# Optimization experiments

Measured on AMD Instinct MI355X. Metric: run time of the kernel, lower is better.

Reference implementation:

```python
import jax, jax.numpy as jnp
import numpy as np

NQ = 4            # num_qubits
DIM = 2 ** NQ     # 16-dim complex state

def _rx(theta):
    c = jnp.cos(theta / 2.0); s = jnp.sin(theta / 2.0)
    return jnp.array([[c, -1j * s], [-1j * s, c]], dtype=jnp.complex64)

def _ry(theta):
    c = jnp.cos(theta / 2.0); s = jnp.sin(theta / 2.0)
    return jnp.array([[c, -s], [s, c]], dtype=jnp.complex64)

def _apply_1q(state, q, U):
    # state: [B, 16] complex; apply 2x2 unitary U on qubit q (qubit 0 = MSB)
    B = state.shape[0]
    st = state.reshape((B,) + (2,) * NQ)
    st = jnp.moveaxis(st, 1 + q, -1)
    st = st @ U.T
    st = jnp.moveaxis(st, -1, 1 + q)
    return st.reshape(B, DIM)

def _apply_cnot(state, c, t):
    # flip target qubit t where control qubit c == 1
    B = state.shape[0]
    st = state.reshape((B,) + (2,) * NQ)
    st = jnp.moveaxis(st, (1 + c, 1 + t), (-2, -1))
    st = jnp.stack([st[..., 0, :], st[..., 1, ::-1]], axis=-2)
    st = jnp.moveaxis(st, (-2, -1), (1 + c, 1 + t))
    return st.reshape(B, DIM)

def _circuit(state):
    rx1, ry1 = _rx(0.1), _ry(0.2)
    rx2, ry2 = _rx(0.3), _ry(0.4)
    for q in range(NQ):
        state = _apply_1q(state, q, rx1)
        state = _apply_1q(state, q, ry1)
    for q in range(NQ - 1):
        state = _apply_cnot(state, q, q + 1)
    for q in range(NQ):
        state = _apply_1q(state, q, rx2)
        state = _apply_1q(state, q, ry2)
    return state

def setup_inputs() -> dict:
    key = jax.random.key(0)
    ks = jax.random.split(key, 9)
    B = 65536
    return {
        'x':   jax.random.normal(ks[0], (B, 784), dtype=jnp.float32),
        'We1': jax.random.normal(ks[1], (784, 256), dtype=jnp.float32) * 0.05,
        'be1': jnp.zeros((256,), dtype=jnp.float32),
        'We2': jax.random.normal(ks[2], (256, 32), dtype=jnp.float32) * 0.05,
        'be2': jnp.zeros((32,), dtype=jnp.float32),
        'W1':  jax.random.normal(ks[3], (32, 128), dtype=jnp.float32) * 0.05,
        'b1':  jnp.zeros((128,), dtype=jnp.float32),
        'W2':  jax.random.normal(ks[4], (128, 10), dtype=jnp.float32) * 0.05,
        'b2':  jnp.zeros((10,), dtype=jnp.float32),
    }

def reference(x, We1, be1, We2, be2, W1, b1, W2, b2):
    # encoder: Linear(784,256) -> ReLU -> Linear(256,32) -> Tanh
    h = jax.nn.relu(x @ We1 + be1)
    enc = jnp.tanh(h @ We2 + be2)               # [B, 32]
    psi = (enc[:, :DIM] + 1j * enc[:, DIM:]).astype(jnp.complex64)
    norm = jnp.sqrt(jnp.sum(jnp.abs(psi) ** 2, axis=1, keepdims=True))
    psi = psi / norm
    psi = _circuit(psi)                          # [B, 16] complex
    feat = jnp.concatenate([psi.real, psi.imag], axis=1)  # [B, 32]
    # classifier: Linear(32,128) -> ReLU -> (Dropout=identity in eval) -> Linear(128,10)
    out = jax.nn.relu(feat @ W1 + b1) @ W2 + b2
    return out
```

## Files before the change

kernel.cpp:

```cpp
#include <hip/hip_runtime.h>
#include <stdint.h>

#define DEVINL __device__ __forceinline__

typedef short bf16x8 __attribute__((ext_vector_type(8)));
typedef float f32x4  __attribute__((ext_vector_type(4)));

DEVINL uint16_t f2bf(float f) {
    uint32_t u = __builtin_bit_cast(uint32_t, f);
    uint32_t r = u + 0x7fffu + ((u >> 16) & 1u);
    return (uint16_t)(r >> 16);
}

DEVINL f32x4 mfma16x16x32(bf16x8 a, bf16x8 b, f32x4 c) {
    return __builtin_amdgcn_mfma_f32_16x16x32_bf16(a, b, c, 0, 0, 0);
}

DEVINL void async_load16(const void* g, void* l) {
    __builtin_amdgcn_global_load_lds(
        (const __attribute__((address_space(1))) void*)g,
        (__attribute__((address_space(3))) void*)l, 16, 0, 0);
}

#define WS_WE1T 0
#define WS_WE2T 425984
#define WS_W1T  442368
#define WS_W2T  450560

__global__ __launch_bounds__(256) void prep_weights(
    const float* __restrict__ We1, const float* __restrict__ We2,
    const float* __restrict__ W1,  const float* __restrict__ W2,
    uint16_t* __restrict__ We1T, uint16_t* __restrict__ We2T,
    uint16_t* __restrict__ W1T,  uint16_t* __restrict__ W2T) {
    int tid = blockIdx.x * 256 + threadIdx.x;
    if (tid < 256 * 832) {
        int n = tid / 832, k = tid % 832;
        We1T[tid] = (k < 784) ? f2bf(We1[k * 256 + n]) : (uint16_t)0;
        return;
    }
    int t2 = tid - 256 * 832;
    if (t2 < 32 * 256) {
        int n = t2 / 256, k = t2 % 256;
        We2T[t2] = f2bf(We2[k * 32 + n]);
        return;
    }
    int t3 = t2 - 32 * 256;
    if (t3 < 128 * 32) {
        int n = t3 / 32, k = t3 % 32;
        W1T[t3] = f2bf(W1[k * 128 + n]);
        return;
    }
    int t4 = t3 - 128 * 32;
    if (t4 < 16 * 128) {
        int n = t4 / 128, k = t4 % 128;
        W2T[t4] = (n < 10) ? f2bf(W2[k * 10 + n]) : (uint16_t)0;
        return;
    }
}

DEVINL void apply_rx(float* sr, float* si, int bit, float c, float s) {
    #pragma unroll
    for (int i = 0; i < 16; i++) {
        if (!(i & bit)) {
            int j = i | bit;
            float r0 = sr[i], i0 = si[i], r1 = sr[j], i1 = si[j];
            sr[i] = c * r0 + s * i1;  si[i] = c * i0 - s * r1;
            sr[j] = c * r1 + s * i0;  si[j] = c * i1 - s * r0;
        }
    }
}
DEVINL void apply_ry(float* sr, float* si, int bit, float c, float s) {
    #pragma unroll
    for (int i = 0; i < 16; i++) {
        if (!(i & bit)) {
            int j = i | bit;
            float r0 = sr[i], i0 = si[i], r1 = sr[j], i1 = si[j];
            sr[i] = c * r0 - s * r1;  si[i] = c * i0 - s * i1;
            sr[j] = s * r0 + c * r1;  si[j] = s * i0 + c * i1;
        }
    }
}
DEVINL void apply_cnot(float* sr, float* si, int cb, int tb) {
    #pragma unroll
    for (int i = 0; i < 16; i++) {
        if ((i & cb) && !(i & tb)) {
            int j = i | tb;
            float tr = sr[i]; sr[i] = sr[j]; sr[j] = tr;
            float ti = si[i]; si[i] = si[j]; si[j] = ti;
        }
    }
}
DEVINL void circuit(float* sr, float* si) {
    const float C1 = 0.99875026039496628f, S1 = 0.04997916927067833f;
    const float C2 = 0.99500416527802582f, S2 = 0.09983341664682815f;
    const float C3 = 0.98877107793604227f, S3 = 0.14943813247359922f;
    const float C4 = 0.98006657784124163f, S4 = 0.19866933079506122f;
    #pragma unroll
    for (int q = 0; q < 4; q++) {
        int bit = 8 >> q;
        apply_rx(sr, si, bit, C1, S1);
        apply_ry(sr, si, bit, C2, S2);
    }
    apply_cnot(sr, si, 8, 4);
    apply_cnot(sr, si, 4, 2);
    apply_cnot(sr, si, 2, 1);
    #pragma unroll
    for (int q = 0; q < 4; q++) {
        int bit = 8 >> q;
        apply_rx(sr, si, bit, C3, S3);
        apply_ry(sr, si, bit, C4, S4);
    }
}

DEVINL void stage_B(const uint16_t* __restrict__ We1T, int k0, uint16_t* Bls, int t) {
    #pragma unroll
    for (int j = 0; j < 8; j++) {
        int g  = j * 256 + t;
        int br = g >> 3;
        int bc = ((g & 7) ^ (br & 7)) * 8;
        async_load16(We1T + (size_t)br * 832 + k0 + bc, &Bls[8 * g]);
    }
}

DEVINL void pack_A(const float4* va, uint16_t* Als, int ar, int ach0, int ach1) {
    union { uint4 u4; uint16_t us[8]; } p0, p1;
    p0.us[0] = f2bf(va[0].x); p0.us[1] = f2bf(va[0].y);
    p0.us[2] = f2bf(va[0].z); p0.us[3] = f2bf(va[0].w);
    p0.us[4] = f2bf(va[1].x); p0.us[5] = f2bf(va[1].y);
    p0.us[6] = f2bf(va[1].z); p0.us[7] = f2bf(va[1].w);
    p1.us[0] = f2bf(va[2].x); p1.us[1] = f2bf(va[2].y);
    p1.us[2] = f2bf(va[2].z); p1.us[3] = f2bf(va[2].w);
    p1.us[4] = f2bf(va[3].x); p1.us[5] = f2bf(va[3].y);
    p1.us[6] = f2bf(va[3].z); p1.us[7] = f2bf(va[3].w);
    *(uint4*)&Als[ar * 64 + ach0 * 8] = p0.u4;
    *(uint4*)&Als[ar * 64 + ach1 * 8] = p1.u4;
}

DEVINL void load_va(float4* va, const float* __restrict__ xrow, int k0, int ac) {
    #pragma unroll
    for (int j = 0; j < 4; j++) {
        int c = k0 + ac + j * 4;
        c = (c <= 780) ? c : 780;
        va[j] = *(const float4*)(xrow + c);
    }
}

DEVINL void compute_tile(const uint16_t* Als, const uint16_t* Bls,
                         f32x4 (&acc)[4][4], int w, int lm, int lq) {
    #pragma unroll
    for (int kk = 0; kk < 2; kk++) {
        bf16x8 afr[4], bfr[4];
        #pragma unroll
        for (int mi = 0; mi < 4; mi++) {
            int row = mi * 16 + lm;
            int ch  = (kk * 4 + lq) ^ (lm & 7);
            afr[mi] = *(const bf16x8*)&Als[row * 64 + ch * 8];
        }
        #pragma unroll
        for (int ni = 0; ni < 4; ni++) {
            int row = w * 64 + ni * 16 + lm;
            int ch  = (kk * 4 + lq) ^ (lm & 7);
            bfr[ni] = *(const bf16x8*)&Bls[row * 64 + ch * 8];
        }
        __builtin_amdgcn_s_setprio(1);
        #pragma unroll
        for (int mi = 0; mi < 4; mi++)
            #pragma unroll
            for (int ni = 0; ni < 4; ni++)
                acc[mi][ni] = mfma16x16x32(afr[mi], bfr[ni], acc[mi][ni]);
        __builtin_amdgcn_s_setprio(0);
    }
}

__global__ __launch_bounds__(256, 2) void fused_kernel(
    const float* __restrict__ x, const uint16_t* __restrict__ We1T,
    const float* __restrict__ be1,
    const uint16_t* __restrict__ We2T, const float* __restrict__ be2,
    const uint16_t* __restrict__ W1T, const float* __restrict__ b1,
    const uint16_t* __restrict__ W2T, const float* __restrict__ b2,
    float* __restrict__ out) {
    __shared__ __align__(16) char smem[81920];
    uint16_t* Htile = (uint16_t*)smem;
    float*    encls  = (float*)smem;
    uint16_t* featls = (uint16_t*)(smem + 8448);
    uint16_t* a1ls   = (uint16_t*)(smem + 13568);

    const int t = threadIdx.x;
    const int rowbase = blockIdx.x * 64;
    const int w  = t >> 6;
    const int l  = t & 63;
    const int lm = l & 15;
    const int lq = l >> 4;

    f32x4 acc[4][4] = {};

    const int ar = t >> 2;
    const int ac = (t & 3) * 16;
    const float* xrow = x + (size_t)(rowbase + ar) * 784;
    const int ach0 = ((t & 3) * 2)     ^ (ar & 7);
    const int ach1 = ((t & 3) * 2 + 1) ^ (ar & 7);

    float4 va[4];

    load_va(va, xrow, 0, ac);
    stage_B(We1T, 0, (uint16_t*)(smem + 8192), t);
    __builtin_amdgcn_sched_barrier(0);
    pack_A(va, (uint16_t*)smem, ar, ach0, ach1);
    load_va(va, xrow, 64, ac);
    asm volatile("s_waitcnt lgkmcnt(0)" ::: "memory");
    asm volatile("s_waitcnt vmcnt(4)" ::: "memory");
    __builtin_amdgcn_s_barrier();
    asm volatile("" ::: "memory");

    int cur = 0;
    for (int it = 0; it < 12; ++it) {
        char* bc = smem + cur * 40960;
        char* bn = smem + (cur ^ 1) * 40960;
        stage_B(We1T, (it + 1) * 64, (uint16_t*)(bn + 8192), t);
        __builtin_amdgcn_sched_barrier(0);
        pack_A(va, (uint16_t*)bn, ar, ach0, ach1);
        load_va(va, xrow, (it + 2) * 64, ac);
        compute_tile((const uint16_t*)bc, (const uint16_t*)(bc + 8192), acc, w, lm, lq);
        asm volatile("s_waitcnt lgkmcnt(0)" ::: "memory");
        asm volatile("s_waitcnt vmcnt(4)" ::: "memory");
        __builtin_amdgcn_s_barrier();
        asm volatile("" ::: "memory");
        cur ^= 1;
    }
    {
        char* bc = smem + cur * 40960;
        compute_tile((const uint16_t*)bc, (const uint16_t*)(bc + 8192), acc, w, lm, lq);
    }

    __syncthreads();

    #pragma unroll
    for (int ni = 0; ni < 4; ni++) {
        int n = w * 64 + ni * 16 + lm;
        float bias = be1[n];
        #pragma unroll
        for (int mi = 0; mi < 4; mi++) {
            #pragma unroll
            for (int i = 0; i < 4; i++) {
                int r = mi * 16 + lq * 4 + i;
                float v = acc[mi][ni][i] + bias;
                v = v > 0.f ? v : 0.f;
                Htile[r * 272 + n] = f2bf(v);
            }
        }
    }
    __syncthreads();

    f32x4 acc2[2] = {};
    #pragma unroll
    for (int k0 = 0; k0 < 256; k0 += 32) {
        bf16x8 af = *(const bf16x8*)&Htile[(w * 16 + lm) * 272 + k0 + lq * 8];
        #pragma unroll
        for (int ni = 0; ni < 2; ni++) {
            bf16x8 bf = *(const bf16x8*)&We2T[(ni * 16 + lm) * 256 + k0 + lq * 8];
            acc2[ni] = mfma16x16x32(af, bf, acc2[ni]);
        }
    }
    __syncthreads();

    #pragma unroll
    for (int ni = 0; ni < 2; ni++) {
        int col = ni * 16 + lm;
        float bias = be2[col];
        #pragma unroll
        for (int i = 0; i < 4; i++) {
            int r = w * 16 + lq * 4 + i;
            encls[r * 33 + col] = tanhf(acc2[ni][i] + bias);
        }
    }
    __syncthreads();

    if (t < 64) {
        float e[32];
        #pragma unroll
        for (int j = 0; j < 32; j++) e[j] = encls[t * 33 + j];
        float s = 0.f;
        #pragma unroll
        for (int j = 0; j < 32; j++) s += e[j] * e[j];
        float inv = 1.0f / sqrtf(s);
        float sr[16], si[16];
        #pragma unroll
        for (int i = 0; i < 16; i++) { sr[i] = e[i] * inv; si[i] = e[16 + i] * inv; }
        circuit(sr, si);
        #pragma unroll
        for (int i = 0; i < 16; i++) {
            featls[t * 40 + i]      = f2bf(sr[i]);
            featls[t * 40 + 16 + i] = f2bf(si[i]);
        }
    }
    __syncthreads();

    f32x4 acc3[8] = {};
    {
        bf16x8 af = *(const bf16x8*)&featls[(w * 16 + lm) * 40 + lq * 8];
        #pragma unroll
        for (int ni = 0; ni < 8; ni++) {
            bf16x8 bf = *(const bf16x8*)&W1T[(ni * 16 + lm) * 32 + lq * 8];
            acc3[ni] = mfma16x16x32(af, bf, acc3[ni]);
        }
    }
    #pragma unroll
    for (int ni = 0; ni < 8; ni++) {
        int col = ni * 16 + lm;
        float bias = b1[col];
        #pragma unroll
        for (int i = 0; i < 4; i++) {
            int r = w * 16 + lq * 4 + i;
            float v = acc3[ni][i] + bias;
            v = v > 0.f ? v : 0.f;
            a1ls[r * 136 + col] = f2bf(v);
        }
    }

    f32x4 acc4 = {};
    #pragma unroll
    for (int k0 = 0; k0 < 128; k0 += 32) {
        bf16x8 af = *(const bf16x8*)&a1ls[(w * 16 + lm) * 136 + k0 + lq * 8];
        bf16x8 bf = *(const bf16x8*)&W2T[lm * 128 + k0 + lq * 8];
        acc4 = mfma16x16x32(af, bf, acc4);
    }
    if (lm < 10) {
        float bias = b2[lm];
        #pragma unroll
        for (int i = 0; i < 4; i++) {
            int r = rowbase + w * 16 + lq * 4 + i;
            out[(size_t)r * 10 + lm] = acc4[i] + bias;
        }
    }
}

extern "C" void kernel_launch(void* const* d_in, const int* in_sizes, int n_in,
                              void* d_out, int out_size, void* d_ws, size_t ws_size,
                              hipStream_t stream) {
    const float* x   = (const float*)d_in[0];
    const float* We1 = (const float*)d_in[1];
    const float* be1 = (const float*)d_in[2];
    const float* We2 = (const float*)d_in[3];
    const float* be2 = (const float*)d_in[4];
    const float* W1  = (const float*)d_in[5];
    const float* b1  = (const float*)d_in[6];
    const float* W2  = (const float*)d_in[7];
    const float* b2  = (const float*)d_in[8];
    float* out = (float*)d_out;

    char* ws = (char*)d_ws;
    uint16_t* We1T = (uint16_t*)(ws + WS_WE1T);
    uint16_t* We2T = (uint16_t*)(ws + WS_WE2T);
    uint16_t* W1T  = (uint16_t*)(ws + WS_W1T);
    uint16_t* W2T  = (uint16_t*)(ws + WS_W2T);

    hipLaunchKernelGGL(prep_weights, dim3(888), dim3(256), 0, stream,
                       We1, We2, W1, W2, We1T, We2T, W1T, W2T);
    hipLaunchKernelGGL(fused_kernel, dim3(1024), dim3(256), 0, stream,
                       x, We1T, be1, We2T, be2, W1T, b1, W2T, b2, out);
}
```

Measured before the change: 324.7 us.

## Pre-swizzle weights into MFMA fragment order and read B directly from global

The weight prep kernel now writes all four bf16 weight matrices in per-lane MFMA fragment order. The main GEMM loop loads B operands straight from global or L2 with coalesced 16-byte loads, instead of staging We1 tiles through LDS with async loads. This cuts LDS to only the A (x) double buffer, shrinking shared memory from 80KB to 34KB and raising launch bounds to 4 blocks per CU for more occupancy. The cost is that every wave re-reads its B slice from cache, with global-load latency now exposed inside the MFMA loop. The x prefetch is restructured into a two-register-buffer pipeline over a fully unrolled loop.

```diff
diff --git a/kernel.cpp b/kernel.cpp
--- a/kernel.cpp
+++ b/kernel.cpp
@@ -16,44 +16,58 @@
     return __builtin_amdgcn_mfma_f32_16x16x32_bf16(a, b, c, 0, 0, 0);
 }
 
-DEVINL void async_load16(const void* g, void* l) {
-    __builtin_amdgcn_global_load_lds(
-        (const __attribute__((address_space(1))) void*)g,
-        (__attribute__((address_space(3))) void*)l, 16, 0, 0);
-}
-
-#define WS_WE1T 0
-#define WS_WE2T 425984
-#define WS_W1T  442368
-#define WS_W2T  450560
+#define WS_BF1 0
+#define WS_BF2 425984
+#define WS_BF3 442368
+#define WS_BF4 450560
 
 __global__ __launch_bounds__(256) void prep_weights(
     const float* __restrict__ We1, const float* __restrict__ We2,
     const float* __restrict__ W1,  const float* __restrict__ W2,
-    uint16_t* __restrict__ We1T, uint16_t* __restrict__ We2T,
-    uint16_t* __restrict__ W1T,  uint16_t* __restrict__ W2T) {
+    uint16_t* __restrict__ Bf1, uint16_t* __restrict__ Bf2,
+    uint16_t* __restrict__ Bf3, uint16_t* __restrict__ Bf4) {
     int tid = blockIdx.x * 256 + threadIdx.x;
-    if (tid < 256 * 832) {
-        int n = tid / 832, k = tid % 832;
-        We1T[tid] = (k < 784) ? f2bf(We1[k * 256 + n]) : (uint16_t)0;
+    if (tid < 212992) {
+        int e    = tid & 7;
+        int lane = (tid >> 3) & 63;
+        int ni   = (tid >> 9) & 3;
+        int kk   = (tid >> 11) & 1;
+        int w    = (tid >> 12) & 3;
+        int step = tid >> 14;
+        int n = w * 64 + ni * 16 + (lane & 15);
+        int k = step * 64 + kk * 32 + (lane >> 4) * 8 + e;
+        Bf1[tid] = (k < 784) ? f2bf(We1[k * 256 + n]) : (uint16_t)0;
         return;
     }
-    int t2 = tid - 256 * 832;
-    if (t2 < 32 * 256) {
-        int n = t2 / 256, k = t2 % 256;
-        We2T[t2] = f2bf(We2[k * 32 + n]);
+    int t2 = tid - 212992;
+    if (t2 < 8192) {
+        int e    = t2 & 7;
+        int lane = (t2 >> 3) & 63;
+        int ni   = (t2 >> 9) & 1;
+        int k0s  = t2 >> 10;
+        int n = ni * 16 + (lane & 15);
+        int k = k0s * 32 + (lane >> 4) * 8 + e;
+        Bf2[t2] = f2bf(We2[k * 32 + n]);
         return;
     }
-    int t3 = t2 - 32 * 256;
-    if (t3 < 128 * 32) {
-        int n = t3 / 32, k = t3 % 32;
-        W1T[t3] = f2bf(W1[k * 128 + n]);
+    int t3 = t2 - 8192;
+    if (t3 < 4096) {
+        int e    = t3 & 7;
+        int lane = (t3 >> 3) & 63;
+        int ni   = t3 >> 9;
+        int n = ni * 16 + (lane & 15);
+        int k = (lane >> 4) * 8 + e;
+        Bf3[t3] = f2bf(W1[k * 128 + n]);
         return;
     }
-    int t4 = t3 - 128 * 32;
-    if (t4 < 16 * 128) {
-        int n = t4 / 128, k = t4 % 128;
-        W2T[t4] = (n < 10) ? f2bf(W2[k * 10 + n]) : (uint16_t)0;
+    int t4 = t3 - 4096;
+    if (t4 < 2048) {
+        int e    = t4 & 7;
+        int lane = (t4 >> 3) & 63;
+        int k0s  = t4 >> 9;
+        int n = lane & 15;
+        int k = k0s * 32 + (lane >> 4) * 8 + e;
+        Bf4[t4] = (n < 10) ? f2bf(W2[k * 10 + n]) : (uint16_t)0;
         return;
     }
 }
@@ -109,16 +123,6 @@
         int bit = 8 >> q;
         apply_rx(sr, si, bit, C3, S3);
         apply_ry(sr, si, bit, C4, S4);
-    }
-}
-
-DEVINL void stage_B(const uint16_t* __restrict__ We1T, int k0, uint16_t* Bls, int t) {
-    #pragma unroll
-    for (int j = 0; j < 8; j++) {
-        int g  = j * 256 + t;
-        int br = g >> 3;
-        int bc = ((g & 7) ^ (br & 7)) * 8;
-        async_load16(We1T + (size_t)br * 832 + k0 + bc, &Bls[8 * g]);
     }
 }
 
@@ -145,22 +149,18 @@
     }
 }
 
-DEVINL void compute_tile(const uint16_t* Als, const uint16_t* Bls,
-                         f32x4 (&acc)[4][4], int w, int lm, int lq) {
+DEVINL void compute_tile(const uint16_t* Als, const uint16_t* __restrict__ Bf,
+                         f32x4 (&acc)[4][4], int l, int lm, int lq) {
     #pragma unroll
     for (int kk = 0; kk < 2; kk++) {
         bf16x8 afr[4], bfr[4];
         #pragma unroll
+        for (int ni = 0; ni < 4; ni++)
+            bfr[ni] = *(const bf16x8*)&Bf[(kk * 4 + ni) * 512 + l * 8];
+        #pragma unroll
         for (int mi = 0; mi < 4; mi++) {
-            int row = mi * 16 + lm;
-            int ch  = (kk * 4 + lq) ^ (lm & 7);
-            afr[mi] = *(const bf16x8*)&Als[row * 64 + ch * 8];
-        }
-        #pragma unroll
-        for (int ni = 0; ni < 4; ni++) {
-            int row = w * 64 + ni * 16 + lm;
-            int ch  = (kk * 4 + lq) ^ (lm & 7);
-            bfr[ni] = *(const bf16x8*)&Bls[row * 64 + ch * 8];
+            int ch = (kk * 4 + lq) ^ (lm & 7);
+            afr[mi] = *(const bf16x8*)&Als[(mi * 16 + lm) * 64 + ch * 8];
         }
         __builtin_amdgcn_s_setprio(1);
         #pragma unroll
@@ -172,14 +172,15 @@
     }
 }
 
-__global__ __launch_bounds__(256, 2) void fused_kernel(
-    const float* __restrict__ x, const uint16_t* __restrict__ We1T,
+__global__ __launch_bounds__(256, 4) void fused_kernel(
+    const float* __restrict__ x, const uint16_t* __restrict__ Bf1,
     const float* __restrict__ be1,
-    const uint16_t* __restrict__ We2T, const float* __restrict__ be2,
-    const uint16_t* __restrict__ W1T, const float* __restrict__ b1,
-    const uint16_t* __restrict__ W2T, const float* __restrict__ b2,
+    const uint16_t* __restrict__ Bf2, const float* __restrict__ be2,
+    const uint16_t* __restrict__ Bf3, const float* __restrict__ b1,
+    const uint16_t* __restrict__ Bf4, const float* __restrict__ b2,
     float* __restrict__ out) {
-    __shared__ __align__(16) char smem[81920];
+    __shared__ __align__(16) char smem[34816];
+    uint16_t* Abuf[2] = { (uint16_t*)smem, (uint16_t*)(smem + 8192) };
     uint16_t* Htile = (uint16_t*)smem;
     float*    encls  = (float*)smem;
     uint16_t* featls = (uint16_t*)(smem + 8448);
@@ -200,36 +201,26 @@
     const int ach0 = ((t & 3) * 2)     ^ (ar & 7);
     const int ach1 = ((t & 3) * 2 + 1) ^ (ar & 7);
 
-    float4 va[4];
-
-    load_va(va, xrow, 0, ac);
-    stage_B(We1T, 0, (uint16_t*)(smem + 8192), t);
-    __builtin_amdgcn_sched_barrier(0);
-    pack_A(va, (uint16_t*)smem, ar, ach0, ach1);
-    load_va(va, xrow, 64, ac);
+    float4 v[2][4];
+
+    load_va(v[0], xrow, 0,   ac);
+    load_va(v[1], xrow, 64,  ac);
+    pack_A(v[0], Abuf[0], ar, ach0, ach1);
+    load_va(v[0], xrow, 128, ac);
     asm volatile("s_waitcnt lgkmcnt(0)" ::: "memory");
-    asm volatile("s_waitcnt vmcnt(4)" ::: "memory");
     __builtin_amdgcn_s_barrier();
-    asm volatile("" ::: "memory");
-
-    int cur = 0;
-    for (int it = 0; it < 12; ++it) {
-        char* bc = smem + cur * 40960;
-        char* bn = smem + (cur ^ 1) * 40960;
-        stage_B(We1T, (it + 1) * 64, (uint16_t*)(bn + 8192), t);
-        __builtin_amdgcn_sched_barrier(0);
-        pack_A(va, (uint16_t*)bn, ar, ach0, ach1);
-        load_va(va, xrow, (it + 2) * 64, ac);
-        compute_tile((const uint16_t*)bc, (const uint16_t*)(bc + 8192), acc, w, lm, lq);
+    __builtin_amdgcn_sched_barrier(0x7F);
+
+    #pragma unroll
+    for (int it = 0; it < 13; ++it) {
+        if (it < 12)
+            pack_A(v[(it + 1) & 1], Abuf[(it + 1) & 1], ar, ach0, ach1);
+        if (it < 10)
+            load_va(v[(it + 1) & 1], xrow, (it + 3) * 64, ac);
+        compute_tile(Abuf[it & 1], Bf1 + (size_t)(it * 4 + w) * 4096, acc, l, lm, lq);
         asm volatile("s_waitcnt lgkmcnt(0)" ::: "memory");
-        asm volatile("s_waitcnt vmcnt(4)" ::: "memory");
         __builtin_amdgcn_s_barrier();
-        asm volatile("" ::: "memory");
-        cur ^= 1;
-    }
-    {
-        char* bc = smem + cur * 40960;
-        compute_tile((const uint16_t*)bc, (const uint16_t*)(bc + 8192), acc, w, lm, lq);
+        __builtin_amdgcn_sched_barrier(0x7F);
     }
 
     __syncthreads();
@@ -243,9 +234,9 @@
             #pragma unroll
             for (int i = 0; i < 4; i++) {
                 int r = mi * 16 + lq * 4 + i;
-                float v = acc[mi][ni][i] + bias;
-                v = v > 0.f ? v : 0.f;
-                Htile[r * 272 + n] = f2bf(v);
+                float v2 = acc[mi][ni][i] + bias;
+                v2 = v2 > 0.f ? v2 : 0.f;
+                Htile[r * 272 + n] = f2bf(v2);
             }
         }
     }
@@ -257,7 +248,7 @@
         bf16x8 af = *(const bf16x8*)&Htile[(w * 16 + lm) * 272 + k0 + lq * 8];
         #pragma unroll
         for (int ni = 0; ni < 2; ni++) {
-            bf16x8 bf = *(const bf16x8*)&We2T[(ni * 16 + lm) * 256 + k0 + lq * 8];
+            bf16x8 bf = *(const bf16x8*)&Bf2[((k0 >> 5) * 2 + ni) * 512 + l * 8];
             acc2[ni] = mfma16x16x32(af, bf, acc2[ni]);
         }
     }
@@ -300,7 +291,7 @@
         bf16x8 af = *(const bf16x8*)&featls[(w * 16 + lm) * 40 + lq * 8];
         #pragma unroll
         for (int ni = 0; ni < 8; ni++) {
-            bf16x8 bf = *(const bf16x8*)&W1T[(ni * 16 + lm) * 32 + lq * 8];
+            bf16x8 bf = *(const bf16x8*)&Bf3[ni * 512 + l * 8];
             acc3[ni] = mfma16x16x32(af, bf, acc3[ni]);
         }
     }
@@ -311,9 +302,9 @@
         #pragma unroll
         for (int i = 0; i < 4; i++) {
             int r = w * 16 + lq * 4 + i;
-            float v = acc3[ni][i] + bias;
-            v = v > 0.f ? v : 0.f;
-            a1ls[r * 136 + col] = f2bf(v);
+            float v2 = acc3[ni][i] + bias;
+            v2 = v2 > 0.f ? v2 : 0.f;
+            a1ls[r * 136 + col] = f2bf(v2);
         }
     }
 
@@ -321,7 +312,7 @@
     #pragma unroll
     for (int k0 = 0; k0 < 128; k0 += 32) {
         bf16x8 af = *(const bf16x8*)&a1ls[(w * 16 + lm) * 136 + k0 + lq * 8];
-        bf16x8 bf = *(const bf16x8*)&W2T[lm * 128 + k0 + lq * 8];
+        bf16x8 bf = *(const bf16x8*)&Bf4[(k0 >> 5) * 512 + l * 8];
         acc4 = mfma16x16x32(af, bf, acc4);
     }
     if (lm < 10) {
@@ -349,13 +340,13 @@
     float* out = (float*)d_out;
 
     char* ws = (char*)d_ws;
-    uint16_t* We1T = (uint16_t*)(ws + WS_WE1T);
-    uint16_t* We2T = (uint16_t*)(ws + WS_WE2T);
-    uint16_t* W1T  = (uint16_t*)(ws + WS_W1T);
-    uint16_t* W2T  = (uint16_t*)(ws + WS_W2T);
+    uint16_t* Bf1 = (uint16_t*)(ws + WS_BF1);
+    uint16_t* Bf2 = (uint16_t*)(ws + WS_BF2);
+    uint16_t* Bf3 = (uint16_t*)(ws + WS_BF3);
+    uint16_t* Bf4 = (uint16_t*)(ws + WS_BF4);
 
     hipLaunchKernelGGL(prep_weights, dim3(888), dim3(256), 0, stream,
-                       We1, We2, W1, W2, We1T, We2T, W1T, W2T);
+                       We1, We2, W1, W2, Bf1, Bf2, Bf3, Bf4);
     hipLaunchKernelGGL(fused_kernel, dim3(1024), dim3(256), 0, stream,
-                       x, We1T, be1, We2T, be2, W1T, b1, W2T, b2, out);
-}
+                       x, Bf1, be1, Bf2, be2, Bf3, b1, Bf4, b2, out);
+}
```

After: 343.1 us. +5.7%, slower.
